# Optimization experiments

Hardware: AMD Instinct MI355X
Metric: run time of the kernel (lower is better)

Reference implementation:

```python
import jax, jax.numpy as jnp
import numpy as np

N_NODES = 50000
N_EDGES = 600000
N_GRAPHS = 256


def gcn_conv(x, W, b, src, dst, n):
    # PyG GCNConv: out = D^{-1/2} (A + I) D^{-1/2} X W + b
    h = x @ W  # [N, out]
    deg = jax.ops.segment_sum(jnp.ones((src.shape[0],), h.dtype), dst, num_segments=n) + 1.0  # self-loop
    dinv = jax.lax.rsqrt(deg)  # deg >= 1 so safe
    msgs = h[src] * (dinv[src] * dinv[dst])[:, None]  # [E, out]
    agg = jax.ops.segment_sum(msgs, dst, num_segments=n)
    agg = agg + h * (dinv * dinv)[:, None]  # self-loop contribution
    return agg + b


def setup_inputs() -> dict:
    key = jax.random.key(0)
    ks = jax.random.split(key, 8)
    x = jax.random.normal(ks[0], (N_NODES, 1), dtype=jnp.float32)
    edge_index = jax.random.randint(ks[1], (2, N_EDGES), 0, N_NODES, dtype=jnp.int64)
    batch = jnp.sort(jax.random.randint(ks[2], (N_NODES,), 0, N_GRAPHS, dtype=jnp.int64))

    def glorot(k, shape):
        lim = np.sqrt(6.0 / (shape[0] + shape[1]))
        return jax.random.uniform(k, shape, jnp.float32, -lim, lim)

    return {
        "x": x,
        "W1": glorot(ks[3], (1, 64)), "b1": jnp.zeros((64,), jnp.float32),
        "W2": glorot(ks[4], (64, 128)), "b2": jnp.zeros((128,), jnp.float32),
        "W3": glorot(ks[5], (128, 64)), "b3": jnp.zeros((64,), jnp.float32),
        "lin1_w": glorot(ks[6], (64, 32)), "lin1_b": jnp.zeros((32,), jnp.float32),
        "lin2_w": glorot(ks[7], (32, 1)), "lin2_b": jnp.zeros((1,), jnp.float32),
        "edge_index": edge_index,
        "batch": batch,
    }


def reference(x, W1, b1, W2, b2, W3, b3, lin1_w, lin1_b, lin2_w, lin2_b, edge_index, batch):
    src, dst = edge_index[0], edge_index[1]
    n = x.shape[0]
    h = jax.nn.relu(gcn_conv(x, W1, b1, src, dst, n))
    h = jax.nn.relu(gcn_conv(h, W2, b2, src, dst, n))
    h = jax.nn.relu(gcn_conv(h, W3, b3, src, dst, n))
    # global_mean_pool
    sums = jax.ops.segment_sum(h, batch, num_segments=N_GRAPHS)
    cnts = jax.ops.segment_sum(jnp.ones((n,), h.dtype), batch, num_segments=N_GRAPHS)
    pooled = sums / jnp.maximum(cnts, 1.0)[:, None]  # [G, 64]
    z = jax.nn.relu(pooled @ lin1_w + lin1_b)
    return z @ lin2_w + lin2_b  # [G, 1]
```

## Files before the change

kernel.cpp:

```cpp
#include <hip/hip_runtime.h>
#include <hip/hip_fp16.h>


#define N_FEAT 64
#define POOL_SUB 16
#define SLOT 64

typedef _Float16 f16x4 __attribute__((ext_vector_type(4)));
typedef float f32x4 __attribute__((ext_vector_type(4)));

__global__ void fill_kernel(const int* __restrict__ src, const int* __restrict__ dst,
                            int* __restrict__ deg, unsigned short* __restrict__ csr, int E) {
    int e4 = (blockIdx.x * blockDim.x + threadIdx.x) * 4;
    if (e4 + 3 < E) {
        int4 sv = *(const int4*)&src[e4];
        int4 dv = *(const int4*)&dst[e4];
        int p0 = atomicAdd(&deg[dv.x], 1);
        int p1 = atomicAdd(&deg[dv.y], 1);
        int p2 = atomicAdd(&deg[dv.z], 1);
        int p3 = atomicAdd(&deg[dv.w], 1);
        csr[dv.x * SLOT + p0] = (unsigned short)sv.x;
        csr[dv.y * SLOT + p1] = (unsigned short)sv.y;
        csr[dv.z * SLOT + p2] = (unsigned short)sv.z;
        csr[dv.w * SLOT + p3] = (unsigned short)sv.w;
    } else {
        for (int e = e4; e < E; ++e) {
            int d = dst[e];
            int pos = atomicAdd(&deg[d], 1);
            csr[d * SLOT + pos] = (unsigned short)src[e];
        }
    }
}

__global__ void prep_kernel(const int* __restrict__ deg, const float* __restrict__ x,
                            float* __restrict__ dinv, float* __restrict__ xd,
                            const float* __restrict__ W2, const float* __restrict__ W3,
                            __half* __restrict__ W2p, __half* __restrict__ W3p, int N) {
    int i = blockIdx.x * blockDim.x + threadIdx.x;
    if (i < N) {
        float dv = rsqrtf((float)deg[i] + 1.0f);
        dinv[i] = dv;
        xd[i] = x[i] * dv;
    }
    if (i < 16384) {
        if (i < 8192) {
            int ii = i & 3;
            int lane = (i >> 2) & 63;
            int blk = i >> 8;
            int k = (blk & 3) * 16 + (lane >> 4) * 4 + ii;
            int col = (blk >> 2) * 16 + (lane & 15);
            W2p[i] = __float2half(W2[k * 128 + col]);
        } else {
            int t2 = i - 8192;
            int ii = t2 & 3;
            int lane = (t2 >> 2) & 63;
            int blk = t2 >> 8;
            int k = (blk & 7) * 16 + (lane >> 4) * 4 + ii;
            int col = (blk >> 3) * 16 + (lane & 15);
            W3p[t2] = __float2half(W3[k * 64 + col]);
        }
    }
}

__global__ void sagg_gather(const int* __restrict__ deg, const unsigned short* __restrict__ csr,
                            const float* __restrict__ xd, const float* __restrict__ dinv,
                            float2* __restrict__ sd, int N) {
    int wid = (blockIdx.x * blockDim.x + threadIdx.x) >> 6;
    int lane = threadIdx.x & 63;
    int v = wid * 4 + (lane >> 4);
    int sub = lane & 15;
    if (v >= N) return;
    int dg = deg[v];
    int base = v * SLOT;
    float sum = 0.0f;
    for (int j = sub; j < dg; j += 16) sum += xd[csr[base + j]];
    #pragma unroll
    for (int off = 8; off; off >>= 1) sum += __shfl_xor(sum, off);
    if (sub == 0) {
        float dv = dinv[v];
        sd[v] = make_float2(dv * (sum + xd[v]), dv);
    }
}

__global__ void agg1_gather(const int* __restrict__ deg, const unsigned short* __restrict__ csr,
                            const float2* __restrict__ sd,
                            const float* __restrict__ W1, const float* __restrict__ b1,
                            __half* __restrict__ agg16, int N) {
    int wave = (blockIdx.x * blockDim.x + threadIdx.x) >> 6;
    int lane = threadIdx.x & 63;
    int v = wave * 2 + (lane >> 5);
    int sub = lane & 31;
    if (v >= N) return;
    float2 w  = *(const float2*)&W1[sub * 2];
    float2 bb = *(const float2*)&b1[sub * 2];
    int dg = deg[v];
    int base = v * SLOT;
    float ax = 0.0f, ay = 0.0f;
    int j = 0;
    for (; j + 3 < dg; j += 4) {
        ushort4 u = *(const ushort4*)&csr[base + j];
        float2 p0 = sd[u.x];
        float2 p1 = sd[u.y];
        float2 p2 = sd[u.z];
        float2 p3 = sd[u.w];
        ax += fmaxf(p0.x * w.x + bb.x, 0.0f) * p0.y + fmaxf(p1.x * w.x + bb.x, 0.0f) * p1.y;
        ax += fmaxf(p2.x * w.x + bb.x, 0.0f) * p2.y + fmaxf(p3.x * w.x + bb.x, 0.0f) * p3.y;
        ay += fmaxf(p0.x * w.y + bb.y, 0.0f) * p0.y + fmaxf(p1.x * w.y + bb.y, 0.0f) * p1.y;
        ay += fmaxf(p2.x * w.y + bb.y, 0.0f) * p2.y + fmaxf(p3.x * w.y + bb.y, 0.0f) * p3.y;
    }
    for (; j < dg; ++j) {
        float2 p = sd[csr[base + j]];
        ax += fmaxf(p.x * w.x + bb.x, 0.0f) * p.y;
        ay += fmaxf(p.x * w.y + bb.y, 0.0f) * p.y;
    }
    float2 pv = sd[v];
    float dv = pv.y;
    float ox = dv * ax + fmaxf(pv.x * w.x + bb.x, 0.0f) * dv * dv;
    float oy = dv * ay + fmaxf(pv.x * w.y + bb.y, 0.0f) * dv * dv;
    *(__half2*)&agg16[(size_t)v * N_FEAT + sub * 2] = __floats2half2_rn(ox, oy);
}

#define H2PAD 136
__global__ __launch_bounds__(256) void gemm12(const __half* __restrict__ A16,
                                              const __half* __restrict__ W2p,
                                              const float* __restrict__ bias2,
                                              const __half* __restrict__ W3p,
                                              const float* __restrict__ dinv,
                                              __half* __restrict__ md, int M) {
    __shared__ __half h2s[32 * H2PAD];
    int tid = threadIdx.x;
    int wave = tid >> 6, lane = tid & 63;
    int g = lane >> 4, r = lane & 15;
    int row0 = blockIdx.x * 32;

    f16x4 af[2][4];
    #pragma unroll
    for (int rt = 0; rt < 2; ++rt) {
        int row = row0 + rt * 16 + r;
        if (row >= M) row = M - 1;
        const __half* ap = A16 + (size_t)row * 64 + g * 4;
        #pragma unroll
        for (int kc = 0; kc < 4; ++kc)
            af[rt][kc] = *(const f16x4*)(ap + kc * 16);
    }

    f32x4 acc[2][2] = {};
    const f16x4* w2v = (const f16x4*)W2p;
    #pragma unroll
    for (int ctl = 0; ctl < 2; ++ctl) {
        int ct = wave * 2 + ctl;
        #pragma unroll
        for (int kc = 0; kc < 4; ++kc) {
            f16x4 bf = w2v[(ct * 4 + kc) * 64 + lane];
            acc[0][ctl] = __builtin_amdgcn_mfma_f32_16x16x16f16(af[0][kc], bf, acc[0][ctl], 0, 0, 0);
            acc[1][ctl] = __builtin_amdgcn_mfma_f32_16x16x16f16(af[1][kc], bf, acc[1][ctl], 0, 0, 0);
        }
    }
    #pragma unroll
    for (int ctl = 0; ctl < 2; ++ctl) {
        int col = (wave * 2 + ctl) * 16 + r;
        float bb = bias2[col];
        #pragma unroll
        for (int rt = 0; rt < 2; ++rt)
            #pragma unroll
            for (int i = 0; i < 4; ++i)
                h2s[(rt * 16 + g * 4 + i) * H2PAD + col] =
                    __float2half(fmaxf(acc[rt][ctl][i] + bb, 0.f));
    }
    __syncthreads();

    f32x4 acc2[2] = {};
    const f16x4* w3v = (const f16x4*)W3p;
    #pragma unroll
    for (int kc = 0; kc < 8; ++kc) {
        f16x4 bf = w3v[(wave * 8 + kc) * 64 + lane];
        #pragma unroll
        for (int rt = 0; rt < 2; ++rt) {
            f16x4 a2 = *(const f16x4*)&h2s[(rt * 16 + r) * H2PAD + kc * 16 + g * 4];
            acc2[rt] = __builtin_amdgcn_mfma_f32_16x16x16f16(a2, bf, acc2[rt], 0, 0, 0);
        }
    }
    #pragma unroll
    for (int rt = 0; rt < 2; ++rt)
        #pragma unroll
        for (int i = 0; i < 4; ++i) {
            int row = row0 + rt * 16 + g * 4 + i;
            if (row < M)
                md[(size_t)row * 64 + wave * 16 + r] = __float2half(acc2[rt][i] * dinv[row]);
        }
}

__global__ void agg3_gather(const int* __restrict__ deg, const unsigned short* __restrict__ csr,
                            const __half* __restrict__ md, const float* __restrict__ dinv,
                            __half* __restrict__ aggh, int N) {
    int wave = (blockIdx.x * blockDim.x + threadIdx.x) >> 6;
    int lane = threadIdx.x & 63;
    int v = wave * 8 + (lane >> 3);
    int sub = lane & 7;
    if (v >= N) return;
    const uint4* mdp = (const uint4*)md;
    int dg = deg[v];
    int base = v * SLOT;
    float a0, a1, a2, a3, a4, a5, a6, a7;
    {
        uint4 sv = mdp[(size_t)v * 8 + sub];
        float2 f0 = __half22float2(*(const __half2*)&sv.x);
        float2 f1 = __half22float2(*(const __half2*)&sv.y);
        float2 f2 = __half22float2(*(const __half2*)&sv.z);
        float2 f3 = __half22float2(*(const __half2*)&sv.w);
        a0 = f0.x; a1 = f0.y; a2 = f1.x; a3 = f1.y;
        a4 = f2.x; a5 = f2.y; a6 = f3.x; a7 = f3.y;
    }
    int j = 0;
    for (; j + 3 < dg; j += 4) {
        ushort4 u = *(const ushort4*)&csr[base + j];
        uint4 x0 = mdp[(size_t)u.x * 8 + sub];
        uint4 x1 = mdp[(size_t)u.y * 8 + sub];
        uint4 x2 = mdp[(size_t)u.z * 8 + sub];
        uint4 x3 = mdp[(size_t)u.w * 8 + sub];
        #define ACC8(X) { \
            float2 t0 = __half22float2(*(const __half2*)&X.x); \
            float2 t1 = __half22float2(*(const __half2*)&X.y); \
            float2 t2 = __half22float2(*(const __half2*)&X.z); \
            float2 t3 = __half22float2(*(const __half2*)&X.w); \
            a0 += t0.x; a1 += t0.y; a2 += t1.x; a3 += t1.y;    \
            a4 += t2.x; a5 += t2.y; a6 += t3.x; a7 += t3.y; }
        ACC8(x0) ACC8(x1) ACC8(x2) ACC8(x3)
    }
    for (; j < dg; ++j) {
        uint4 xv = mdp[(size_t)csr[base + j] * 8 + sub];
        ACC8(xv)
        #undef ACC8
    }
    float dv = dinv[v];
    __half2 o0 = __floats2half2_rn(a0 * dv, a1 * dv);
    __half2 o1 = __floats2half2_rn(a2 * dv, a3 * dv);
    __half2 o2 = __floats2half2_rn(a4 * dv, a5 * dv);
    __half2 o3 = __floats2half2_rn(a6 * dv, a7 * dv);
    uint4 ov = make_uint4(*(unsigned*)&o0, *(unsigned*)&o1, *(unsigned*)&o2, *(unsigned*)&o3);
    *(uint4*)&aggh[(size_t)v * N_FEAT + sub * 8] = ov;
}

__global__ void pool_kernel(const __half* __restrict__ aggh, const float* __restrict__ b3,
                            const int* __restrict__ batch, float* __restrict__ pooled,
                            float* __restrict__ counts, int N) {
    int wave = (blockIdx.x * blockDim.x + threadIdx.x) >> 6;
    int lane = threadIdx.x & 63;
    int start = wave * POOL_SUB;
    if (start >= N) return;
    int end = min(start + POOL_SUB, N);
    float bl = b3[lane];
    int cur = batch[start];
    float acc = 0.0f;
    float cnt = 0.0f;
    for (int i = start; i < end; ++i) {
        int g = batch[i];
        if (g != cur) {
            atomicAdd(&pooled[cur * N_FEAT + lane], acc);
            if (lane == 0) atomicAdd(&counts[cur], cnt);
            acc = 0.0f; cnt = 0.0f; cur = g;
        }
        acc += fmaxf(__half2float(aggh[(size_t)i * N_FEAT + lane]) + bl, 0.0f);
        cnt += 1.0f;
    }
    atomicAdd(&pooled[cur * N_FEAT + lane], acc);
    if (lane == 0) atomicAdd(&counts[cur], cnt);
}

__global__ void mlp_kernel(const float* __restrict__ pooled, const float* __restrict__ counts,
                           const float* __restrict__ l1w, const float* __restrict__ l1b,
                           const float* __restrict__ l2w, const float* __restrict__ l2b,
                           float* __restrict__ out) {
    __shared__ float row[64];
    __shared__ float zs[32];
    int g = blockIdx.x;
    int l = threadIdx.x;
    float cnt = fmaxf(counts[g], 1.0f);
    row[l] = pooled[g * 64 + l] / cnt;
    __syncthreads();
    if (l < 32) {
        float z = l1b[l];
        #pragma unroll
        for (int k = 0; k < 64; ++k) z += row[k] * l1w[k * 32 + l];
        zs[l] = fmaxf(z, 0.0f);
    }
    __syncthreads();
    if (l == 0) {
        float o = l2b[0];
        #pragma unroll
        for (int j = 0; j < 32; ++j) o += zs[j] * l2w[j];
        out[g] = o;
    }
}

extern "C" void kernel_launch(void* const* d_in, const int* in_sizes, int n_in,
                              void* d_out, int out_size, void* d_ws, size_t ws_size,
                              hipStream_t stream) {
    const float* x   = (const float*)d_in[0];
    const float* W1  = (const float*)d_in[1];
    const float* b1  = (const float*)d_in[2];
    const float* W2  = (const float*)d_in[3];
    const float* b2  = (const float*)d_in[4];
    const float* W3  = (const float*)d_in[5];
    const float* b3  = (const float*)d_in[6];
    const float* l1w = (const float*)d_in[7];
    const float* l1b = (const float*)d_in[8];
    const float* l2w = (const float*)d_in[9];
    const float* l2b = (const float*)d_in[10];
    const int* ei    = (const int*)d_in[11];
    const int* batch = (const int*)d_in[12];

    int N = in_sizes[0];
    int E = in_sizes[11] / 2;
    int G = out_size;
    const int* src = ei;
    const int* dst = ei + E;

    char* wsb = (char*)d_ws;
    int*   deg      = (int*)wsb;                 wsb += (size_t)N * 4;
    float* pooled   = (float*)wsb;               wsb += (size_t)G * 64 * 4;
    float* counts   = (float*)wsb;               wsb += (size_t)G * 4;
    unsigned short* csr = (unsigned short*)wsb;  wsb += (size_t)N * SLOT * 2;
    float* dinv     = (float*)wsb;               wsb += (size_t)N * 4;
    float* xd       = (float*)wsb;               wsb += (size_t)N * 4;
    float2* sd      = (float2*)wsb;              wsb += (size_t)N * 8;
    __half* md      = (__half*)wsb;              wsb += (size_t)N * 64 * 2;
    __half* aggh    = (__half*)wsb;              wsb += (size_t)N * 64 * 2;
    __half* agg16   = (__half*)wsb;              wsb += ((size_t)N + 32) * 64 * 2;
    __half* W2p     = (__half*)wsb;              wsb += 8192 * 2;
    __half* W3p     = (__half*)wsb;              wsb += 8192 * 2;

    hipMemsetAsync(deg, 0, ((size_t)N + (size_t)G * 64 + G) * 4, stream);

    int tb = 256;
    fill_kernel<<<(E / 4 + tb - 1) / tb, tb, 0, stream>>>(src, dst, deg, csr, E);
    prep_kernel<<<(N + tb - 1) / tb, tb, 0, stream>>>(deg, x, dinv, xd, W2, W3, W2p, W3p, N);
    sagg_gather<<<((N + 3) / 4 + 3) / 4, tb, 0, stream>>>(deg, csr, xd, dinv, sd, N);
    int a1_waves = (N + 1) / 2;
    agg1_gather<<<(a1_waves + 3) / 4, tb, 0, stream>>>(deg, csr, sd, W1, b1, agg16, N);
    gemm12<<<(N + 31) / 32, tb, 0, stream>>>(agg16, W2p, b2, W3p, dinv, md, N);
    int a3_waves = (N + 7) / 8;
    agg3_gather<<<(a3_waves + 3) / 4, tb, 0, stream>>>(deg, csr, md, dinv, aggh, N);
    int pool_waves = (N + POOL_SUB - 1) / POOL_SUB;
    pool_kernel<<<(pool_waves + 3) / 4, tb, 0, stream>>>(aggh, b3, batch, pooled, counts, N);
    mlp_kernel<<<G, 64, 0, stream>>>(pooled, counts, l1w, l1b, l2w, l2b, (float*)d_out);
}
```

Measured before the change: 191.6 us.

## Fuse mean pooling and MLP into one per-graph kernel using sorted batch

Replaces the atomic-based pooling kernel and the separate MLP kernel with a single kernel that launches one block per graph. Each block binary-searches the sorted batch array for its node range, reduces the rows with four waves, then runs the two linear layers. This drops one launch, the pooled and counts atomics, and the memset of those buffers. It relies on batch being sorted, and with only 256 blocks of roughly 200 rows each the pooling stage has limited parallelism.

```diff
diff --git a/kernel.cpp b/kernel.cpp
--- a/kernel.cpp
+++ b/kernel.cpp
@@ -3,7 +3,6 @@
 
 
 #define N_FEAT 64
-#define POOL_SUB 16
 #define SLOT 64
 
 typedef _Float16 f16x4 __attribute__((ext_vector_type(4)));
@@ -241,51 +240,50 @@
     *(uint4*)&aggh[(size_t)v * N_FEAT + sub * 8] = ov;
 }
 
-__global__ void pool_kernel(const __half* __restrict__ aggh, const float* __restrict__ b3,
-                            const int* __restrict__ batch, float* __restrict__ pooled,
-                            float* __restrict__ counts, int N) {
-    int wave = (blockIdx.x * blockDim.x + threadIdx.x) >> 6;
-    int lane = threadIdx.x & 63;
-    int start = wave * POOL_SUB;
-    if (start >= N) return;
-    int end = min(start + POOL_SUB, N);
-    float bl = b3[lane];
-    int cur = batch[start];
-    float acc = 0.0f;
-    float cnt = 0.0f;
-    for (int i = start; i < end; ++i) {
-        int g = batch[i];
-        if (g != cur) {
-            atomicAdd(&pooled[cur * N_FEAT + lane], acc);
-            if (lane == 0) atomicAdd(&counts[cur], cnt);
-            acc = 0.0f; cnt = 0.0f; cur = g;
-        }
-        acc += fmaxf(__half2float(aggh[(size_t)i * N_FEAT + lane]) + bl, 0.0f);
-        cnt += 1.0f;
-    }
-    atomicAdd(&pooled[cur * N_FEAT + lane], acc);
-    if (lane == 0) atomicAdd(&counts[cur], cnt);
-}
-
-__global__ void mlp_kernel(const float* __restrict__ pooled, const float* __restrict__ counts,
-                           const float* __restrict__ l1w, const float* __restrict__ l1b,
-                           const float* __restrict__ l2w, const float* __restrict__ l2b,
-                           float* __restrict__ out) {
+__global__ __launch_bounds__(256) void pool_mlp_kernel(
+        const __half* __restrict__ aggh, const float* __restrict__ b3,
+        const int* __restrict__ batch,
+        const float* __restrict__ l1w, const float* __restrict__ l1b,
+        const float* __restrict__ l2w, const float* __restrict__ l2b,
+        float* __restrict__ out, int N) {
+    __shared__ int s_bound[2];
+    __shared__ float red[4][64];
     __shared__ float row[64];
     __shared__ float zs[32];
     int g = blockIdx.x;
-    int l = threadIdx.x;
-    float cnt = fmaxf(counts[g], 1.0f);
-    row[l] = pooled[g * 64 + l] / cnt;
-    __syncthreads();
-    if (l < 32) {
-        float z = l1b[l];
-        #pragma unroll
-        for (int k = 0; k < 64; ++k) z += row[k] * l1w[k * 32 + l];
-        zs[l] = fmaxf(z, 0.0f);
-    }
-    __syncthreads();
-    if (l == 0) {
+    int tid = threadIdx.x;
+    if (tid < 2) {
+        int target = g + tid;
+        int lo = 0, hi = N;
+        while (lo < hi) {
+            int mid = (lo + hi) >> 1;
+            if (batch[mid] < target) lo = mid + 1; else hi = mid;
+        }
+        s_bound[tid] = lo;
+    }
+    __syncthreads();
+    int lo = s_bound[0], hi = s_bound[1];
+    int cnt = hi - lo;
+    int wave = tid >> 6, lane = tid & 63;
+    float bl = b3[lane];
+    float acc = 0.0f;
+    for (int i = lo + wave; i < hi; i += 4)
+        acc += fmaxf(__half2float(aggh[(size_t)i * N_FEAT + lane]) + bl, 0.0f);
+    red[wave][lane] = acc;
+    __syncthreads();
+    if (wave == 0) {
+        float s = red[0][lane] + red[1][lane] + red[2][lane] + red[3][lane];
+        row[lane] = s / fmaxf((float)cnt, 1.0f);
+    }
+    __syncthreads();
+    if (tid < 32) {
+        float z = l1b[tid];
+        #pragma unroll
+        for (int k = 0; k < 64; ++k) z += row[k] * l1w[k * 32 + tid];
+        zs[tid] = fmaxf(z, 0.0f);
+    }
+    __syncthreads();
+    if (tid == 0) {
         float o = l2b[0];
         #pragma unroll
         for (int j = 0; j < 32; ++j) o += zs[j] * l2w[j];
@@ -318,8 +316,6 @@
 
     char* wsb = (char*)d_ws;
     int*   deg      = (int*)wsb;                 wsb += (size_t)N * 4;
-    float* pooled   = (float*)wsb;               wsb += (size_t)G * 64 * 4;
-    float* counts   = (float*)wsb;               wsb += (size_t)G * 4;
     unsigned short* csr = (unsigned short*)wsb;  wsb += (size_t)N * SLOT * 2;
     float* dinv     = (float*)wsb;               wsb += (size_t)N * 4;
     float* xd       = (float*)wsb;               wsb += (size_t)N * 4;
@@ -330,7 +326,7 @@
     __half* W2p     = (__half*)wsb;              wsb += 8192 * 2;
     __half* W3p     = (__half*)wsb;              wsb += 8192 * 2;
 
-    hipMemsetAsync(deg, 0, ((size_t)N + (size_t)G * 64 + G) * 4, stream);
+    hipMemsetAsync(deg, 0, (size_t)N * 4, stream);
 
     int tb = 256;
     fill_kernel<<<(E / 4 + tb - 1) / tb, tb, 0, stream>>>(src, dst, deg, csr, E);
@@ -341,7 +337,6 @@
     gemm12<<<(N + 31) / 32, tb, 0, stream>>>(agg16, W2p, b2, W3p, dinv, md, N);
     int a3_waves = (N + 7) / 8;
     agg3_gather<<<(a3_waves + 3) / 4, tb, 0, stream>>>(deg, csr, md, dinv, aggh, N);
-    int pool_waves = (N + POOL_SUB - 1) / POOL_SUB;
-    pool_kernel<<<(pool_waves + 3) / 4, tb, 0, stream>>>(aggh, b3, batch, pooled, counts, N);
-    mlp_kernel<<<G, 64, 0, stream>>>(pooled, counts, l1w, l1b, l2w, l2b, (float*)d_out);
-}
+    pool_mlp_kernel<<<G, tb, 0, stream>>>(aggh, b3, batch, l1w, l1b, l2w, l2b,
+                                          (float*)d_out, N);
+}
```

After: 196.7 us. 2.6% more time.
